# Performance work log

Measured on AMD Instinct MI355X. Metric: run time of the kernel, lower is better.

## Reference

```python
import jax, jax.numpy as jnp
import numpy as np

H = 1024


def _linear(x, W, b):
    # torch nn.Linear: y = x @ W.T + b
    return jnp.einsum('...i,oi->...o', x, W) + b


def setup_inputs() -> dict:
    key = jax.random.key(0)
    ks = jax.random.split(key, 10)
    s = 1.0 / np.sqrt(H)
    inp = {
        'p': jax.random.normal(ks[0], (8, 4096, H), dtype=jnp.float32),
        'x': jax.random.normal(ks[1], (8, 64, H), dtype=jnp.float32),
        'Wq': jax.random.uniform(ks[2], (H, H), jnp.float32, -s, s),
        'bq': jax.random.uniform(ks[3], (H,), jnp.float32, -s, s),
        'Wk': jax.random.uniform(ks[4], (H, H), jnp.float32, -s, s),
        'bk': jax.random.uniform(ks[5], (H,), jnp.float32, -s, s),
        'Wv': jax.random.uniform(ks[6], (H, H), jnp.float32, -s, s),
        'bv': jax.random.uniform(ks[7], (H,), jnp.float32, -s, s),
        'Wg': jax.random.uniform(ks[8], (1, 2 * H), jnp.float32, -s, s),
        'bg': jax.random.uniform(ks[9], (1,), jnp.float32, -s, s),
    }
    return inp


def reference(p, x, Wq, bq, Wk, bk, Wv, bv, Wg, bg):
    q = _linear(p, Wq, bq)            # (B, S, H)
    k = _linear(x, Wk, bk)            # (B, L, H)
    v = _linear(x, Wv, bv)            # (B, L, H)
    # NOTE: scale applied AFTER softmax, faithful to the original module
    scores = jax.nn.softmax(jnp.einsum('bsh,blh->bsl', q, k), axis=-1)
    scores = scores / jnp.sqrt(jnp.asarray(H, p.dtype))
    out = jnp.einsum('bsl,blh->bsh', scores, v) + p
    g = jax.nn.sigmoid(_linear(jnp.concatenate([out, p], axis=2), Wg, bg))  # (B,S,1)
    return g * out + (1.0 - g) * p
```

## Files before the change

### kernel.cpp

```cpp
#include <hip/hip_runtime.h>

#define H 1024
#define SEQ 4096

typedef float f32x4 __attribute__((ext_vector_type(4)));
typedef short s16x8 __attribute__((ext_vector_type(8)));
typedef unsigned short u16;
typedef u16 u16x4 __attribute__((ext_vector_type(4)));
typedef u16 u16x8 __attribute__((ext_vector_type(8)));

__device__ inline u16 f2bf(float f) {
  union { float f; unsigned u; } v; v.f = f;
  unsigned r = v.u + 0x7fffu + ((v.u >> 16) & 1u);
  return (u16)(r >> 16);
}
__device__ inline float bf2f(u16 b) {
  union { unsigned u; float f; } v; v.u = ((unsigned)b) << 16; return v.f;
}

__device__ __forceinline__ void cvt16(const float* __restrict__ src, u16* __restrict__ dst, int i) {
  const float4* s = reinterpret_cast<const float4*>(src) + (size_t)i * 4;
  float4 a = s[0], b = s[1], c = s[2], d = s[3];
  u16x8 lo, hi;
  lo[0]=f2bf(a.x); lo[1]=f2bf(a.y); lo[2]=f2bf(a.z); lo[3]=f2bf(a.w);
  lo[4]=f2bf(b.x); lo[5]=f2bf(b.y); lo[6]=f2bf(b.z); lo[7]=f2bf(b.w);
  hi[0]=f2bf(c.x); hi[1]=f2bf(c.y); hi[2]=f2bf(c.z); hi[3]=f2bf(c.w);
  hi[4]=f2bf(d.x); hi[5]=f2bf(d.y); hi[6]=f2bf(d.z); hi[7]=f2bf(d.w);
  u16x8* o = reinterpret_cast<u16x8*>(dst) + (size_t)i * 2;
  o[0] = lo; o[1] = hi;
}

__global__ __launch_bounds__(256) void prep_kernel(
    const float* __restrict__ Wq, const float* __restrict__ Wk,
    const float* __restrict__ Wv, const float* __restrict__ x,
    const float* __restrict__ Wg,
    u16* __restrict__ wqTb, u16* __restrict__ wkb, u16* __restrict__ wvb,
    u16* __restrict__ xb, float* __restrict__ wgs, float* __restrict__ zeros) {
  __shared__ u16 tls[64][65];
  int blk = blockIdx.x, t = threadIdx.x;
  if (blk < 256) {
    int ti = blk >> 4, tj = blk & 15;
    int lr = t >> 2, cq = (t & 3) * 16;
    const float* s = Wq + (size_t)(ti * 64 + lr) * H + tj * 64 + cq;
#pragma unroll
    for (int q = 0; q < 4; ++q) {
      float4 v = *reinterpret_cast<const float4*>(s + q * 4);
      tls[lr][cq + q * 4 + 0] = f2bf(v.x);
      tls[lr][cq + q * 4 + 1] = f2bf(v.y);
      tls[lr][cq + q * 4 + 2] = f2bf(v.z);
      tls[lr][cq + q * 4 + 3] = f2bf(v.w);
    }
    __syncthreads();
    u16x8 a, b2;
#pragma unroll
    for (int i = 0; i < 8; ++i) a[i] = tls[cq + i][lr];
#pragma unroll
    for (int i = 0; i < 8; ++i) b2[i] = tls[cq + 8 + i][lr];
    u16* d = wqTb + (size_t)(tj * 64 + lr) * H + ti * 64 + cq;
    *reinterpret_cast<u16x8*>(d) = a;
    *reinterpret_cast<u16x8*>(d + 8) = b2;
  } else if (blk < 512) {
    cvt16(Wk, wkb, (blk - 256) * 256 + t);
  } else if (blk < 768) {
    cvt16(Wv, wvb, (blk - 512) * 256 + t);
  } else if (blk < 896) {
    cvt16(x, xb, (blk - 768) * 256 + t);
  } else {
    int i = t * 4;
    float4 a = *reinterpret_cast<const float4*>(Wg + i);
    float4 b2 = *reinterpret_cast<const float4*>(Wg + H + i);
    float4 o; o.x=a.x+b2.x; o.y=a.y+b2.y; o.z=a.z+b2.z; o.w=a.w+b2.w;
    *reinterpret_cast<float4*>(wgs + i) = o;
    float4 z; z.x=0.f; z.y=0.f; z.z=0.f; z.w=0.f;
    *reinterpret_cast<float4*>(zeros + i) = z;
  }
}

__device__ __forceinline__ void gemm_body(const u16* __restrict__ A, const u16* __restrict__ W,
                                          const float* __restrict__ bias, u16* __restrict__ out,
                                          int mt, int nt, int omode, u16* sm) {
  int m0 = mt * 128, n0 = nt * 128;
  int t = threadIdx.x;
  int wave = t >> 6, lane = t & 63;
  int lane15 = lane & 15, lhi = lane >> 4;
  int wr = wave >> 1, wc = wave & 1;
  u16* a_sm = sm;
  u16* b_sm = sm + 8192;

  f32x4 acc[4][4];
#pragma unroll
  for (int mi = 0; mi < 4; ++mi)
#pragma unroll
    for (int ni = 0; ni < 4; ++ni) acc[mi][ni] = (f32x4)0.f;

  int rsel = wave * 32 + (lane >> 3);
  int csel = (lane & 7) * 8;
  const u16* Ab = A + (size_t)m0 * H + csel;
  const u16* Wb = W + (size_t)n0 * H + csel;

  for (int kt = 0; kt < 16; ++kt) {
    int kc = kt * 64;
#pragma unroll
    for (int j = 0; j < 4; ++j) {
      const u16* ga = Ab + (size_t)(rsel + j * 8) * H + kc;
      const u16* gb = Wb + (size_t)(rsel + j * 8) * H + kc;
      __builtin_amdgcn_global_load_lds((const __attribute__((address_space(1))) unsigned int*)ga,
                                       (__attribute__((address_space(3))) unsigned int*)&a_sm[wave * 2048 + j * 512],
                                       16, 0, 0);
      __builtin_amdgcn_global_load_lds((const __attribute__((address_space(1))) unsigned int*)gb,
                                       (__attribute__((address_space(3))) unsigned int*)&b_sm[wave * 2048 + j * 512],
                                       16, 0, 0);
    }
    __syncthreads();
#pragma unroll
    for (int ks = 0; ks < 2; ++ks) {
      s16x8 af[4], bfr[4];
#pragma unroll
      for (int mi = 0; mi < 4; ++mi)
        af[mi] = *reinterpret_cast<const s16x8*>(&a_sm[(wr * 64 + mi * 16 + lane15) * 64 + ks * 32 + lhi * 8]);
#pragma unroll
      for (int ni = 0; ni < 4; ++ni)
        bfr[ni] = *reinterpret_cast<const s16x8*>(&b_sm[(wc * 64 + ni * 16 + lane15) * 64 + ks * 32 + lhi * 8]);
#pragma unroll
      for (int mi = 0; mi < 4; ++mi)
#pragma unroll
        for (int ni = 0; ni < 4; ++ni)
          acc[mi][ni] = __builtin_amdgcn_mfma_f32_16x16x32_bf16(af[mi], bfr[ni], acc[mi][ni], 0, 0, 0);
    }
    __syncthreads();
  }

  float bqv[4];
#pragma unroll
  for (int ni = 0; ni < 4; ++ni) bqv[ni] = bias[n0 + wc * 64 + ni * 16 + lane15];

  if (omode == 0) {
#pragma unroll
    for (int mi = 0; mi < 4; ++mi)
#pragma unroll
      for (int ni = 0; ni < 4; ++ni)
#pragma unroll
        for (int r = 0; r < 4; ++r)
          sm[(wr * 64 + mi * 16 + lhi * 4 + r) * 128 + wc * 64 + ni * 16 + lane15] =
              f2bf(acc[mi][ni][r] + bqv[ni]);
    __syncthreads();
#pragma unroll
    for (int i = 0; i < 4; ++i) {
      int lin2 = i * 4096 + t * 16;
      int row = lin2 >> 7, col = lin2 & 127;
      u16x8 v0 = *reinterpret_cast<const u16x8*>(&sm[lin2]);
      u16x8 v1 = *reinterpret_cast<const u16x8*>(&sm[lin2 + 8]);
      u16* o = out + (size_t)(m0 + row) * H + n0 + col;
      *reinterpret_cast<u16x8*>(o) = v0;
      *reinterpret_cast<u16x8*>(o + 8) = v1;
    }
  } else {
#pragma unroll
    for (int mi = 0; mi < 4; ++mi)
#pragma unroll
      for (int ni = 0; ni < 4; ++ni) {
        int col = n0 + wc * 64 + ni * 16 + lane15;
#pragma unroll
        for (int r = 0; r < 4; ++r) {
          int row = m0 + wr * 64 + mi * 16 + lhi * 4 + r;
          out[((size_t)(row >> 6) * H + col) * 64 + (row & 63)] = f2bf(acc[mi][ni][r] + bqv[ni]);
        }
      }
  }
}

__global__ __launch_bounds__(256) void kv1_kernel(const u16* __restrict__ xb,
                                                  const u16* __restrict__ wkb, const u16* __restrict__ wvb,
                                                  const float* __restrict__ bk, const float* __restrict__ bv,
                                                  u16* __restrict__ kbf, u16* __restrict__ vTb) {
  __shared__ __align__(16) u16 sm[128 * 128];
  int sel = blockIdx.x >> 5;
  int bid = blockIdx.x & 31;
  if (sel == 0)
    gemm_body(xb, wkb, bk, kbf, bid >> 3, bid & 7, 0, sm);
  else
    gemm_body(xb, wvb, bv, vTb, bid >> 3, bid & 7, 2, sm);
}

__global__ __launch_bounds__(256) void kv2_kernel(const u16* __restrict__ kbf,
                                                  const u16* __restrict__ wqTb,
                                                  const float* __restrict__ zeros,
                                                  u16* __restrict__ ktb,
                                                  const u16* __restrict__ vTb,
                                                  const float* __restrict__ Wg,
                                                  const float* __restrict__ bq,
                                                  float* __restrict__ vg, float* __restrict__ bqk) {
  if (blockIdx.x < 32) {
    __shared__ __align__(16) u16 sm[128 * 128];
    gemm_body(kbf, wqTb, zeros, ktb, blockIdx.x >> 3, blockIdx.x & 7, 0, sm);
  } else {
    __shared__ float bq_s[H];
    __shared__ float partial[4][64];
    int b = blockIdx.x - 32, t = threadIdx.x;
    *reinterpret_cast<float4*>(&bq_s[t * 4]) = *reinterpret_cast<const float4*>(bq + t * 4);
    int l = t & 63, part = t >> 6;
    float s = 0.f;
    const u16* vtp = vTb + ((size_t)b * H + part * 256) * 64 + l;
    for (int h = 0; h < 256; ++h) s += bf2f(vtp[h * 64]) * Wg[part * 256 + h];
    partial[part][l] = s;
    __syncthreads();
    if (t < 64) vg[b * 64 + t] = partial[0][t] + partial[1][t] + partial[2][t] + partial[3][t];
    int row = t >> 2, qp = t & 3;
    const u16* kr = kbf + ((size_t)b * 64 + row) * H + qp * 256;
    float sb = 0.f;
    for (int j = 0; j < 256; j += 8) {
      u16x8 v8 = *reinterpret_cast<const u16x8*>(kr + j);
      const float* bqp = &bq_s[qp * 256 + j];
#pragma unroll
      for (int i2 = 0; i2 < 8; ++i2) sb += bf2f(v8[i2]) * bqp[i2];
    }
    sb += __shfl_xor(sb, 1);
    sb += __shfl_xor(sb, 2);
    if (qp == 0) bqk[b * 64 + row] = sb;
  }
}

__global__ __launch_bounds__(256, 4) void attn_kernel(
    const float* __restrict__ p, const u16* __restrict__ ktb,
    const u16* __restrict__ vT, const float* __restrict__ wgs,
    const float* __restrict__ vg, const float* __restrict__ bqk,
    const float* __restrict__ bg, float* __restrict__ out) {
  int t = threadIdx.x;
  int orig = blockIdx.x;
  int lin = (orig & 7) * 128 + (orig >> 3);
  int b = lin >> 7, st = lin & 127;
  size_t gm0 = (size_t)b * SEQ + (size_t)st * 32;
  int wave = t >> 6, lane = t & 63, lane15 = lane & 15, lhi = lane >> 4;

  __shared__ __align__(16) float Sp[4][2048];
  __shared__ __align__(16) u16 P_lds[32 * 72];
  __shared__ float vg_l[64], bq_l[64], pg_part[4][32], gs_l[32];

  if (t < 64) { vg_l[t] = vg[b * 64 + t]; bq_l[t] = bqk[b * 64 + t]; }

  {
    const float* pb = p + (gm0 + lane15) * H;
    const u16* kb = ktb + ((size_t)b * 64 + lane15) * H;
    int kq = wave * 256 + lhi * 8;

    f32x4 acc[2][4];
#pragma unroll
    for (int mi = 0; mi < 2; ++mi)
#pragma unroll
      for (int ni = 0; ni < 4; ++ni) acc[mi][ni] = (f32x4)0.f;
    float pg0 = 0.f, pg1 = 0.f;

#pragma unroll 1
    for (int kt = 0; kt < 8; ++kt) {
      int kc = kq + kt * 32;
      f32x4 p0a = *reinterpret_cast<const f32x4*>(pb + kc);
      f32x4 p0b = *reinterpret_cast<const f32x4*>(pb + kc + 4);
      f32x4 p1a = *reinterpret_cast<const f32x4*>(pb + 16 * H + kc);
      f32x4 p1b = *reinterpret_cast<const f32x4*>(pb + 16 * H + kc + 4);
      s16x8 kf0 = *reinterpret_cast<const s16x8*>(kb + kc);
      s16x8 kf1 = *reinterpret_cast<const s16x8*>(kb + 16 * H + kc);
      s16x8 kf2 = *reinterpret_cast<const s16x8*>(kb + 32 * H + kc);
      s16x8 kf3 = *reinterpret_cast<const s16x8*>(kb + 48 * H + kc);
      f32x4 w0 = *reinterpret_cast<const f32x4*>(wgs + kc);
      f32x4 w1 = *reinterpret_cast<const f32x4*>(wgs + kc + 4);

      s16x8 a0, a1;
      a0[0]=f2bf(p0a[0]); a0[1]=f2bf(p0a[1]); a0[2]=f2bf(p0a[2]); a0[3]=f2bf(p0a[3]);
      a0[4]=f2bf(p0b[0]); a0[5]=f2bf(p0b[1]); a0[6]=f2bf(p0b[2]); a0[7]=f2bf(p0b[3]);
      a1[0]=f2bf(p1a[0]); a1[1]=f2bf(p1a[1]); a1[2]=f2bf(p1a[2]); a1[3]=f2bf(p1a[3]);
      a1[4]=f2bf(p1b[0]); a1[5]=f2bf(p1b[1]); a1[6]=f2bf(p1b[2]); a1[7]=f2bf(p1b[3]);

      acc[0][0] = __builtin_amdgcn_mfma_f32_16x16x32_bf16(a0, kf0, acc[0][0], 0, 0, 0);
      acc[0][1] = __builtin_amdgcn_mfma_f32_16x16x32_bf16(a0, kf1, acc[0][1], 0, 0, 0);
      acc[0][2] = __builtin_amdgcn_mfma_f32_16x16x32_bf16(a0, kf2, acc[0][2], 0, 0, 0);
      acc[0][3] = __builtin_amdgcn_mfma_f32_16x16x32_bf16(a0, kf3, acc[0][3], 0, 0, 0);
      acc[1][0] = __builtin_amdgcn_mfma_f32_16x16x32_bf16(a1, kf0, acc[1][0], 0, 0, 0);
      acc[1][1] = __builtin_amdgcn_mfma_f32_16x16x32_bf16(a1, kf1, acc[1][1], 0, 0, 0);
      acc[1][2] = __builtin_amdgcn_mfma_f32_16x16x32_bf16(a1, kf2, acc[1][2], 0, 0, 0);
      acc[1][3] = __builtin_amdgcn_mfma_f32_16x16x32_bf16(a1, kf3, acc[1][3], 0, 0, 0);

      pg0 += p0a[0]*w0[0] + p0a[1]*w0[1] + p0a[2]*w0[2] + p0a[3]*w0[3]
           + p0b[0]*w1[0] + p0b[1]*w1[1] + p0b[2]*w1[2] + p0b[3]*w1[3];
      pg1 += p1a[0]*w0[0] + p1a[1]*w0[1] + p1a[2]*w0[2] + p1a[3]*w0[3]
           + p1b[0]*w1[0] + p1b[1]*w1[1] + p1b[2]*w1[2] + p1b[3]*w1[3];
    }

    pg0 += __shfl_xor(pg0, 16); pg0 += __shfl_xor(pg0, 32);
    pg1 += __shfl_xor(pg1, 16); pg1 += __shfl_xor(pg1, 32);
    if (lane < 16) { pg_part[wave][lane15] = pg0; pg_part[wave][16 + lane15] = pg1; }

    float* sp = &Sp[wave][0];
#pragma unroll
    for (int mi = 0; mi < 2; ++mi)
#pragma unroll
      for (int ni = 0; ni < 4; ++ni)
#pragma unroll
        for (int r = 0; r < 4; ++r)
          sp[(mi * 16 + lhi * 4 + r) * 64 + ni * 16 + lane15] = acc[mi][ni][r];
  }
  __syncthreads();

  {
    int row = t >> 3, c0 = (t & 7) * 8;
    f32x4 sA = (f32x4)0.f, sB = (f32x4)0.f;
#pragma unroll
    for (int w = 0; w < 4; ++w) {
      sA += *reinterpret_cast<const f32x4*>(&Sp[w][row * 64 + c0]);
      sB += *reinterpret_cast<const f32x4*>(&Sp[w][row * 64 + c0 + 4]);
    }
    float ev[8];
    float se = 0.f, sv = 0.f;
#pragma unroll
    for (int j = 0; j < 4; ++j) {
      float e = __expf(sA[j] + bq_l[c0 + j]);
      ev[j] = e; se += e; sv += e * vg_l[c0 + j];
    }
#pragma unroll
    for (int j = 0; j < 4; ++j) {
      float e = __expf(sB[j] + bq_l[c0 + 4 + j]);
      ev[4 + j] = e; se += e; sv += e * vg_l[c0 + 4 + j];
    }
    se += __shfl_xor(se, 1); se += __shfl_xor(se, 2); se += __shfl_xor(se, 4);
    sv += __shfl_xor(sv, 1); sv += __shfl_xor(sv, 2); sv += __shfl_xor(sv, 4);
    u16x8 pw;
#pragma unroll
    for (int j = 0; j < 8; ++j) pw[j] = f2bf(ev[j]);
    *reinterpret_cast<u16x8*>(&P_lds[row * 72 + c0]) = pw;
    if ((t & 7) == 0) {
      float pg = pg_part[0][row] + pg_part[1][row] + pg_part[2][row] + pg_part[3][row];
      float inv = 1.f / (32.f * se);
      float logit = sv * inv + pg + bg[0];
      gs_l[row] = inv / (1.f + __expf(-logit));
    }
  }
  __syncthreads();

  {
    s16x8 pa[2][2];
#pragma unroll
    for (int mi = 0; mi < 2; ++mi)
#pragma unroll
      for (int ks = 0; ks < 2; ++ks)
        pa[mi][ks] = *reinterpret_cast<const s16x8*>(&P_lds[(mi * 16 + lane15) * 72 + ks * 32 + lhi * 8]);

    const u16* vb = vT + (size_t)b * H * 64;
    float* sc = &Sp[0][0] + wave * 2048;
#pragma unroll
    for (int hcc = 0; hcc < 4; ++hcc) {
      int hbase = wave * 256 + hcc * 64;
      f32x4 acc[2][4];
#pragma unroll
      for (int mi = 0; mi < 2; ++mi)
#pragma unroll
        for (int ni = 0; ni < 4; ++ni) acc[mi][ni] = (f32x4)0.f;
#pragma unroll
      for (int ks = 0; ks < 2; ++ks) {
        s16x8 bv8[4];
#pragma unroll
        for (int ni = 0; ni < 4; ++ni)
          bv8[ni] = *reinterpret_cast<const s16x8*>(vb + (size_t)(hbase + ni * 16 + lane15) * 64 + ks * 32 + lhi * 8);
#pragma unroll
        for (int mi = 0; mi < 2; ++mi)
#pragma unroll
          for (int ni = 0; ni < 4; ++ni)
            acc[mi][ni] = __builtin_amdgcn_mfma_f32_16x16x32_bf16(pa[mi][ks], bv8[ni], acc[mi][ni], 0, 0, 0);
      }
      int swz = (lhi & 1) << 4;
#pragma unroll
      for (int mi = 0; mi < 2; ++mi)
#pragma unroll
        for (int ni = 0; ni < 4; ++ni)
#pragma unroll
          for (int r = 0; r < 4; ++r)
            sc[(mi * 16 + lhi * 4 + r) * 64 + ((ni * 16 + lane15) ^ swz)] = acc[mi][ni][r];
      asm volatile("s_waitcnt lgkmcnt(0)" ::: "memory");
      __builtin_amdgcn_sched_barrier(0);
#pragma unroll
      for (int ii = 0; ii < 8; ++ii) {
        int flat4 = ii * 64 + lane;
        int lrow = flat4 >> 4;
        int c4 = flat4 & 15;
        int scol = (c4 * 4) ^ (((lrow >> 2) & 1) << 4);
        f32x4 a = *reinterpret_cast<const f32x4*>(&sc[lrow * 64 + scol]);
        size_t grow = gm0 + lrow;
        float f = gs_l[lrow];
        float4 pr4 = *reinterpret_cast<const float4*>(&p[grow * H + hbase + c4 * 4]);
        f32x4 o;
        o[0] = pr4.x + f * a[0];
        o[1] = pr4.y + f * a[1];
        o[2] = pr4.z + f * a[2];
        o[3] = pr4.w + f * a[3];
        *reinterpret_cast<f32x4*>(&out[grow * H + hbase + c4 * 4]) = o;
      }
      asm volatile("s_waitcnt lgkmcnt(0)" ::: "memory");
    }
  }
}

extern "C" void kernel_launch(void* const* d_in, const int* in_sizes, int n_in,
                              void* d_out, int out_size, void* d_ws, size_t ws_size,
                              hipStream_t stream) {
  const float* p  = (const float*)d_in[0];
  const float* x  = (const float*)d_in[1];
  const float* Wq = (const float*)d_in[2];
  const float* bq = (const float*)d_in[3];
  const float* Wk = (const float*)d_in[4];
  const float* bk = (const float*)d_in[5];
  const float* Wv = (const float*)d_in[6];
  const float* bv = (const float*)d_in[7];
  const float* Wg = (const float*)d_in[8];
  const float* bg = (const float*)d_in[9];
  float* out = (float*)d_out;

  char* ws = (char*)d_ws;
  u16* wqTb    = (u16*)(ws);
  u16* wkb     = (u16*)(ws + 2097152);
  u16* wvb     = (u16*)(ws + 4194304);
  u16* xb      = (u16*)(ws + 6291456);
  u16* kbf     = (u16*)(ws + 7340032);
  u16* ktb     = (u16*)(ws + 8388608);
  u16* vTb     = (u16*)(ws + 9437184);
  float* wgs   = (float*)(ws + 10485760);
  float* zeros = (float*)(ws + 10489856);
  float* vg    = (float*)(ws + 10493952);
  float* bqk   = (float*)(ws + 10498048);

  prep_kernel<<<897, 256, 0, stream>>>(Wq, Wk, Wv, x, Wg, wqTb, wkb, wvb, xb, wgs, zeros);
  kv1_kernel<<<64, 256, 0, stream>>>(xb, wkb, wvb, bk, bv, kbf, vTb);
  kv2_kernel<<<40, 256, 0, stream>>>(kbf, wqTb, zeros, ktb, vTb, Wg, bq, vg, bqk);
  attn_kernel<<<1024, 256, 0, stream>>>(p, ktb, vTb, wgs, vg, bqk, bg, out);
}
```

Measured before the change: 126.2 us.

## Stage p tile as bf16 in LDS and reuse it for scores, gate, and residual

The attention kernel now processes 16 query rows per block instead of 32 and launches twice as many blocks. Each block loads its p rows once from global memory, converts them to bf16, and keeps them in a swizzled LDS buffer. That buffer feeds the QK MFMA, the gate dot product and the final residual add, removing the second fp32 read of p from global memory. In exchange the residual and gate now use bf16-rounded p, which loses precision. LDS use per block rises and the launch bound drops to 3 blocks per CU.

```diff
diff --git a/kernel.cpp b/kernel.cpp
--- a/kernel.cpp
+++ b/kernel.cpp
@@ -220,114 +220,108 @@
   }
 }
 
-__global__ __launch_bounds__(256, 4) void attn_kernel(
+__global__ __launch_bounds__(256, 3) void attn_kernel(
     const float* __restrict__ p, const u16* __restrict__ ktb,
     const u16* __restrict__ vT, const float* __restrict__ wgs,
     const float* __restrict__ vg, const float* __restrict__ bqk,
     const float* __restrict__ bg, float* __restrict__ out) {
   int t = threadIdx.x;
   int orig = blockIdx.x;
-  int lin = (orig & 7) * 128 + (orig >> 3);
-  int b = lin >> 7, st = lin & 127;
-  size_t gm0 = (size_t)b * SEQ + (size_t)st * 32;
+  int lin = (orig & 7) * 256 + (orig >> 3);
+  int b = lin >> 8, st = lin & 255;
+  size_t gm0 = (size_t)b * SEQ + (size_t)st * 16;
   int wave = t >> 6, lane = t & 63, lane15 = lane & 15, lhi = lane >> 4;
 
-  __shared__ __align__(16) float Sp[4][2048];
-  __shared__ __align__(16) u16 P_lds[32 * 72];
-  __shared__ float vg_l[64], bq_l[64], pg_part[4][32], gs_l[32];
+  __shared__ __align__(16) u16 p_lds[16 * 1024];
+  __shared__ __align__(16) float Sp[4][1024];
+  __shared__ __align__(16) u16 P_lds[16 * 72];
+  __shared__ float vg_l[64], bq_l[64], gs_l[16];
 
   if (t < 64) { vg_l[t] = vg[b * 64 + t]; bq_l[t] = bqk[b * 64 + t]; }
 
   {
-    const float* pb = p + (gm0 + lane15) * H;
-    const u16* kb = ktb + ((size_t)b * 64 + lane15) * H;
-    int kq = wave * 256 + lhi * 8;
-
-    f32x4 acc[2][4];
-#pragma unroll
-    for (int mi = 0; mi < 2; ++mi)
-#pragma unroll
-      for (int ni = 0; ni < 4; ++ni) acc[mi][ni] = (f32x4)0.f;
-    float pg0 = 0.f, pg1 = 0.f;
+    int srow = t >> 7;
+    int scol = t & 127;
+    const float* gp = p + (gm0 + srow) * H + scol * 8;
+    f32x4 r0[8], r1[8];
+#pragma unroll
+    for (int i = 0; i < 8; ++i) {
+      r0[i] = *reinterpret_cast<const f32x4*>(gp + (size_t)(2 * i) * H);
+      r1[i] = *reinterpret_cast<const f32x4*>(gp + (size_t)(2 * i) * H + 4);
+    }
+#pragma unroll
+    for (int i = 0; i < 8; ++i) {
+      int row = 2 * i + srow;
+      u16x8 o;
+      o[0]=f2bf(r0[i][0]); o[1]=f2bf(r0[i][1]); o[2]=f2bf(r0[i][2]); o[3]=f2bf(r0[i][3]);
+      o[4]=f2bf(r1[i][0]); o[5]=f2bf(r1[i][1]); o[6]=f2bf(r1[i][2]); o[7]=f2bf(r1[i][3]);
+      *reinterpret_cast<u16x8*>(&p_lds[row * 1024 + ((scol ^ (row & 7)) << 3)]) = o;
+    }
+  }
+  __syncthreads();
+
+  {
+    const u16* kb = ktb + ((size_t)b * 64 + lane15) * H + lhi * 8;
+    f32x4 acc[4];
+#pragma unroll
+    for (int ni = 0; ni < 4; ++ni) acc[ni] = (f32x4)0.f;
+    int arow = lane15 * 1024;
+    int aswz = lane15 & 7;
 
 #pragma unroll 1
     for (int kt = 0; kt < 8; ++kt) {
-      int kc = kq + kt * 32;
-      f32x4 p0a = *reinterpret_cast<const f32x4*>(pb + kc);
-      f32x4 p0b = *reinterpret_cast<const f32x4*>(pb + kc + 4);
-      f32x4 p1a = *reinterpret_cast<const f32x4*>(pb + 16 * H + kc);
-      f32x4 p1b = *reinterpret_cast<const f32x4*>(pb + 16 * H + kc + 4);
-      s16x8 kf0 = *reinterpret_cast<const s16x8*>(kb + kc);
-      s16x8 kf1 = *reinterpret_cast<const s16x8*>(kb + 16 * H + kc);
-      s16x8 kf2 = *reinterpret_cast<const s16x8*>(kb + 32 * H + kc);
-      s16x8 kf3 = *reinterpret_cast<const s16x8*>(kb + 48 * H + kc);
-      f32x4 w0 = *reinterpret_cast<const f32x4*>(wgs + kc);
-      f32x4 w1 = *reinterpret_cast<const f32x4*>(wgs + kc + 4);
-
-      s16x8 a0, a1;
-      a0[0]=f2bf(p0a[0]); a0[1]=f2bf(p0a[1]); a0[2]=f2bf(p0a[2]); a0[3]=f2bf(p0a[3]);
-      a0[4]=f2bf(p0b[0]); a0[5]=f2bf(p0b[1]); a0[6]=f2bf(p0b[2]); a0[7]=f2bf(p0b[3]);
-      a1[0]=f2bf(p1a[0]); a1[1]=f2bf(p1a[1]); a1[2]=f2bf(p1a[2]); a1[3]=f2bf(p1a[3]);
-      a1[4]=f2bf(p1b[0]); a1[5]=f2bf(p1b[1]); a1[6]=f2bf(p1b[2]); a1[7]=f2bf(p1b[3]);
-
-      acc[0][0] = __builtin_amdgcn_mfma_f32_16x16x32_bf16(a0, kf0, acc[0][0], 0, 0, 0);
-      acc[0][1] = __builtin_amdgcn_mfma_f32_16x16x32_bf16(a0, kf1, acc[0][1], 0, 0, 0);
-      acc[0][2] = __builtin_amdgcn_mfma_f32_16x16x32_bf16(a0, kf2, acc[0][2], 0, 0, 0);
-      acc[0][3] = __builtin_amdgcn_mfma_f32_16x16x32_bf16(a0, kf3, acc[0][3], 0, 0, 0);
-      acc[1][0] = __builtin_amdgcn_mfma_f32_16x16x32_bf16(a1, kf0, acc[1][0], 0, 0, 0);
-      acc[1][1] = __builtin_amdgcn_mfma_f32_16x16x32_bf16(a1, kf1, acc[1][1], 0, 0, 0);
-      acc[1][2] = __builtin_amdgcn_mfma_f32_16x16x32_bf16(a1, kf2, acc[1][2], 0, 0, 0);
-      acc[1][3] = __builtin_amdgcn_mfma_f32_16x16x32_bf16(a1, kf3, acc[1][3], 0, 0, 0);
-
-      pg0 += p0a[0]*w0[0] + p0a[1]*w0[1] + p0a[2]*w0[2] + p0a[3]*w0[3]
-           + p0b[0]*w1[0] + p0b[1]*w1[1] + p0b[2]*w1[2] + p0b[3]*w1[3];
-      pg1 += p1a[0]*w0[0] + p1a[1]*w0[1] + p1a[2]*w0[2] + p1a[3]*w0[3]
-           + p1b[0]*w1[0] + p1b[1]*w1[1] + p1b[2]*w1[2] + p1b[3]*w1[3];
-    }
-
-    pg0 += __shfl_xor(pg0, 16); pg0 += __shfl_xor(pg0, 32);
-    pg1 += __shfl_xor(pg1, 16); pg1 += __shfl_xor(pg1, 32);
-    if (lane < 16) { pg_part[wave][lane15] = pg0; pg_part[wave][16 + lane15] = pg1; }
-
+      int kc = wave * 256 + kt * 32;
+      int sb = (kc >> 3) + lhi;
+      s16x8 a = *reinterpret_cast<const s16x8*>(&p_lds[arow + ((sb ^ aswz) << 3)]);
+      s16x8 k0 = *reinterpret_cast<const s16x8*>(kb + kc);
+      s16x8 k1 = *reinterpret_cast<const s16x8*>(kb + (size_t)16 * H + kc);
+      s16x8 k2 = *reinterpret_cast<const s16x8*>(kb + (size_t)32 * H + kc);
+      s16x8 k3 = *reinterpret_cast<const s16x8*>(kb + (size_t)48 * H + kc);
+      acc[0] = __builtin_amdgcn_mfma_f32_16x16x32_bf16(a, k0, acc[0], 0, 0, 0);
+      acc[1] = __builtin_amdgcn_mfma_f32_16x16x32_bf16(a, k1, acc[1], 0, 0, 0);
+      acc[2] = __builtin_amdgcn_mfma_f32_16x16x32_bf16(a, k2, acc[2], 0, 0, 0);
+      acc[3] = __builtin_amdgcn_mfma_f32_16x16x32_bf16(a, k3, acc[3], 0, 0, 0);
+    }
     float* sp = &Sp[wave][0];
 #pragma unroll
-    for (int mi = 0; mi < 2; ++mi)
-#pragma unroll
-      for (int ni = 0; ni < 4; ++ni)
-#pragma unroll
-        for (int r = 0; r < 4; ++r)
-          sp[(mi * 16 + lhi * 4 + r) * 64 + ni * 16 + lane15] = acc[mi][ni][r];
+    for (int ni = 0; ni < 4; ++ni)
+#pragma unroll
+      for (int r = 0; r < 4; ++r)
+        sp[(lhi * 4 + r) * 64 + ni * 16 + lane15] = acc[ni][r];
   }
   __syncthreads();
 
   {
-    int row = t >> 3, c0 = (t & 7) * 8;
-    f32x4 sA = (f32x4)0.f, sB = (f32x4)0.f;
-#pragma unroll
-    for (int w = 0; w < 4; ++w) {
-      sA += *reinterpret_cast<const f32x4*>(&Sp[w][row * 64 + c0]);
-      sB += *reinterpret_cast<const f32x4*>(&Sp[w][row * 64 + c0 + 4]);
-    }
-    float ev[8];
-    float se = 0.f, sv = 0.f;
+    int row = t >> 4, q = t & 15;
+    int cq = q * 4;
+    f32x4 s4 = *reinterpret_cast<const f32x4*>(&Sp[0][row * 64 + cq]);
+    s4 += *reinterpret_cast<const f32x4*>(&Sp[1][row * 64 + cq]);
+    s4 += *reinterpret_cast<const f32x4*>(&Sp[2][row * 64 + cq]);
+    s4 += *reinterpret_cast<const f32x4*>(&Sp[3][row * 64 + cq]);
+    float ev[4], se = 0.f, sv = 0.f;
 #pragma unroll
     for (int j = 0; j < 4; ++j) {
-      float e = __expf(sA[j] + bq_l[c0 + j]);
-      ev[j] = e; se += e; sv += e * vg_l[c0 + j];
-    }
-#pragma unroll
-    for (int j = 0; j < 4; ++j) {
-      float e = __expf(sB[j] + bq_l[c0 + 4 + j]);
-      ev[4 + j] = e; se += e; sv += e * vg_l[c0 + 4 + j];
-    }
-    se += __shfl_xor(se, 1); se += __shfl_xor(se, 2); se += __shfl_xor(se, 4);
-    sv += __shfl_xor(sv, 1); sv += __shfl_xor(sv, 2); sv += __shfl_xor(sv, 4);
-    u16x8 pw;
-#pragma unroll
-    for (int j = 0; j < 8; ++j) pw[j] = f2bf(ev[j]);
-    *reinterpret_cast<u16x8*>(&P_lds[row * 72 + c0]) = pw;
-    if ((t & 7) == 0) {
-      float pg = pg_part[0][row] + pg_part[1][row] + pg_part[2][row] + pg_part[3][row];
+      float e = __expf(s4[j] + bq_l[cq + j]);
+      ev[j] = e; se += e; sv += e * vg_l[cq + j];
+    }
+    float pg = 0.f;
+    int prow = row * 1024, pswz = row & 7;
+#pragma unroll
+    for (int k8 = 0; k8 < 8; ++k8) {
+      int s = q * 8 + k8;
+      u16x8 pv8 = *reinterpret_cast<const u16x8*>(&p_lds[prow + ((s ^ pswz) << 3)]);
+      const float* w_ = wgs + q * 64 + k8 * 8;
+      pg += bf2f(pv8[0]) * w_[0] + bf2f(pv8[1]) * w_[1] + bf2f(pv8[2]) * w_[2] + bf2f(pv8[3]) * w_[3]
+          + bf2f(pv8[4]) * w_[4] + bf2f(pv8[5]) * w_[5] + bf2f(pv8[6]) * w_[6] + bf2f(pv8[7]) * w_[7];
+    }
+    se += __shfl_xor(se, 1); se += __shfl_xor(se, 2); se += __shfl_xor(se, 4); se += __shfl_xor(se, 8);
+    sv += __shfl_xor(sv, 1); sv += __shfl_xor(sv, 2); sv += __shfl_xor(sv, 4); sv += __shfl_xor(sv, 8);
+    pg += __shfl_xor(pg, 1); pg += __shfl_xor(pg, 2); pg += __shfl_xor(pg, 4); pg += __shfl_xor(pg, 8);
+    u16x4 pw;
+#pragma unroll
+    for (int j = 0; j < 4; ++j) pw[j] = f2bf(ev[j]);
+    *reinterpret_cast<u16x4*>(&P_lds[row * 72 + cq]) = pw;
+    if (q == 0) {
       float inv = 1.f / (32.f * se);
       float logit = sv * inv + pg + bg[0];
       gs_l[row] = inv / (1.f + __expf(-logit));
@@ -336,23 +330,19 @@
   __syncthreads();
 
   {
-    s16x8 pa[2][2];
-#pragma unroll
-    for (int mi = 0; mi < 2; ++mi)
-#pragma unroll
-      for (int ks = 0; ks < 2; ++ks)
-        pa[mi][ks] = *reinterpret_cast<const s16x8*>(&P_lds[(mi * 16 + lane15) * 72 + ks * 32 + lhi * 8]);
+    s16x8 pa[2];
+#pragma unroll
+    for (int ks = 0; ks < 2; ++ks)
+      pa[ks] = *reinterpret_cast<const s16x8*>(&P_lds[lane15 * 72 + ks * 32 + lhi * 8]);
 
     const u16* vb = vT + (size_t)b * H * 64;
-    float* sc = &Sp[0][0] + wave * 2048;
+    float* sc = &Sp[0][0] + wave * 1024;
 #pragma unroll
     for (int hcc = 0; hcc < 4; ++hcc) {
       int hbase = wave * 256 + hcc * 64;
-      f32x4 acc[2][4];
-#pragma unroll
-      for (int mi = 0; mi < 2; ++mi)
-#pragma unroll
-        for (int ni = 0; ni < 4; ++ni) acc[mi][ni] = (f32x4)0.f;
+      f32x4 acc[4];
+#pragma unroll
+      for (int ni = 0; ni < 4; ++ni) acc[ni] = (f32x4)0.f;
 #pragma unroll
       for (int ks = 0; ks < 2; ++ks) {
         s16x8 bv8[4];
@@ -360,37 +350,34 @@
         for (int ni = 0; ni < 4; ++ni)
           bv8[ni] = *reinterpret_cast<const s16x8*>(vb + (size_t)(hbase + ni * 16 + lane15) * 64 + ks * 32 + lhi * 8);
 #pragma unroll
-        for (int mi = 0; mi < 2; ++mi)
-#pragma unroll
-          for (int ni = 0; ni < 4; ++ni)
-            acc[mi][ni] = __builtin_amdgcn_mfma_f32_16x16x32_bf16(pa[mi][ks], bv8[ni], acc[mi][ni], 0, 0, 0);
+        for (int ni = 0; ni < 4; ++ni)
+          acc[ni] = __builtin_amdgcn_mfma_f32_16x16x32_bf16(pa[ks], bv8[ni], acc[ni], 0, 0, 0);
       }
       int swz = (lhi & 1) << 4;
 #pragma unroll
-      for (int mi = 0; mi < 2; ++mi)
-#pragma unroll
-        for (int ni = 0; ni < 4; ++ni)
-#pragma unroll
-          for (int r = 0; r < 4; ++r)
-            sc[(mi * 16 + lhi * 4 + r) * 64 + ((ni * 16 + lane15) ^ swz)] = acc[mi][ni][r];
+      for (int ni = 0; ni < 4; ++ni)
+#pragma unroll
+        for (int r = 0; r < 4; ++r)
+          sc[(lhi * 4 + r) * 64 + ((ni * 16 + lane15) ^ swz)] = acc[ni][r];
       asm volatile("s_waitcnt lgkmcnt(0)" ::: "memory");
       __builtin_amdgcn_sched_barrier(0);
 #pragma unroll
-      for (int ii = 0; ii < 8; ++ii) {
+      for (int ii = 0; ii < 4; ++ii) {
         int flat4 = ii * 64 + lane;
         int lrow = flat4 >> 4;
         int c4 = flat4 & 15;
         int scol = (c4 * 4) ^ (((lrow >> 2) & 1) << 4);
         f32x4 a = *reinterpret_cast<const f32x4*>(&sc[lrow * 64 + scol]);
-        size_t grow = gm0 + lrow;
-        float f = gs_l[lrow];
-        float4 pr4 = *reinterpret_cast<const float4*>(&p[grow * H + hbase + c4 * 4]);
+        int sres = (hbase >> 3) + (c4 >> 1);
+        u16x4 pr = *reinterpret_cast<const u16x4*>(
+            &p_lds[lrow * 1024 + ((sres ^ (lrow & 7)) << 3) + (c4 & 1) * 4]);
+        float g = gs_l[lrow];
         f32x4 o;
-        o[0] = pr4.x + f * a[0];
-        o[1] = pr4.y + f * a[1];
-        o[2] = pr4.z + f * a[2];
-        o[3] = pr4.w + f * a[3];
-        *reinterpret_cast<f32x4*>(&out[grow * H + hbase + c4 * 4]) = o;
+        o[0] = bf2f(pr[0]) + g * a[0];
+        o[1] = bf2f(pr[1]) + g * a[1];
+        o[2] = bf2f(pr[2]) + g * a[2];
+        o[3] = bf2f(pr[3]) + g * a[3];
+        *reinterpret_cast<f32x4*>(&out[(gm0 + lrow) * H + hbase + c4 * 4]) = o;
       }
       asm volatile("s_waitcnt lgkmcnt(0)" ::: "memory");
     }
@@ -428,5 +415,5 @@
   prep_kernel<<<897, 256, 0, stream>>>(Wq, Wk, Wv, x, Wg, wqTb, wkb, wvb, xb, wgs, zeros);
   kv1_kernel<<<64, 256, 0, stream>>>(xb, wkb, wvb, bk, bv, kbf, vTb);
   kv2_kernel<<<40, 256, 0, stream>>>(kbf, wqTb, zeros, ktb, vTb, Wg, bq, vg, bqk);
-  attn_kernel<<<1024, 256, 0, stream>>>(p, ktb, vTb, wgs, vg, bqk, bg, out);
-}
+  attn_kernel<<<2048, 256, 0, stream>>>(p, ktb, vTb, wgs, vg, bqk, bg, out);
+}
```

Measured after the change: 161.3 us. 27.8% more time.

## Split attention kernel into score/softmax kernel and PV/output kernel

Applied to the files above, without the earlier changes.

Splits the fused attention kernel into two launches. The first computes scores, the softmax weights and the gate, writing bf16 probabilities and gate scales to workspace (reusing the wk/xb regions). The second reads them back, runs the PV MFMA and the residual epilogue. The apparent aim is lighter per-kernel resource use, but the 64 MB p tensor is now read twice from HBM and there is extra launch and global round-trip overhead.

```diff
diff --git a/kernel.cpp b/kernel.cpp
--- a/kernel.cpp
+++ b/kernel.cpp
@@ -220,11 +220,11 @@
   }
 }
 
-__global__ __launch_bounds__(256, 4) void attn_kernel(
+__global__ __launch_bounds__(256, 4) void s_kernel(
     const float* __restrict__ p, const u16* __restrict__ ktb,
-    const u16* __restrict__ vT, const float* __restrict__ wgs,
-    const float* __restrict__ vg, const float* __restrict__ bqk,
-    const float* __restrict__ bg, float* __restrict__ out) {
+    const float* __restrict__ wgs, const float* __restrict__ vg,
+    const float* __restrict__ bqk, const float* __restrict__ bg,
+    u16* __restrict__ Pbuf, float* __restrict__ gsbuf) {
   int t = threadIdx.x;
   int orig = blockIdx.x;
   int lin = (orig & 7) * 128 + (orig >> 3);
@@ -233,8 +233,7 @@
   int wave = t >> 6, lane = t & 63, lane15 = lane & 15, lhi = lane >> 4;
 
   __shared__ __align__(16) float Sp[4][2048];
-  __shared__ __align__(16) u16 P_lds[32 * 72];
-  __shared__ float vg_l[64], bq_l[64], pg_part[4][32], gs_l[32];
+  __shared__ float vg_l[64], bq_l[64], pg_part[4][32];
 
   if (t < 64) { vg_l[t] = vg[b * 64 + t]; bq_l[t] = bqk[b * 64 + t]; }
 
@@ -325,75 +324,91 @@
     u16x8 pw;
 #pragma unroll
     for (int j = 0; j < 8; ++j) pw[j] = f2bf(ev[j]);
-    *reinterpret_cast<u16x8*>(&P_lds[row * 72 + c0]) = pw;
+    *reinterpret_cast<u16x8*>(&Pbuf[(size_t)lin * 2048 + row * 64 + c0]) = pw;
     if ((t & 7) == 0) {
       float pg = pg_part[0][row] + pg_part[1][row] + pg_part[2][row] + pg_part[3][row];
       float inv = 1.f / (32.f * se);
       float logit = sv * inv + pg + bg[0];
-      gs_l[row] = inv / (1.f + __expf(-logit));
-    }
-  }
+      gsbuf[lin * 32 + row] = inv / (1.f + __expf(-logit));
+    }
+  }
+}
+
+__global__ __launch_bounds__(256, 4) void pv_kernel(
+    const float* __restrict__ p, const u16* __restrict__ vT,
+    const u16* __restrict__ Pbuf, const float* __restrict__ gsbuf,
+    float* __restrict__ out) {
+  int t = threadIdx.x;
+  int orig = blockIdx.x;
+  int lin = (orig & 7) * 128 + (orig >> 3);
+  int b = lin >> 7, st = lin & 127;
+  size_t gm0 = (size_t)b * SEQ + (size_t)st * 32;
+  int wave = t >> 6, lane = t & 63, lane15 = lane & 15, lhi = lane >> 4;
+
+  __shared__ __align__(16) float sc_all[4][2048];
+  __shared__ float gs_l[32];
+
+  if (t < 32) gs_l[t] = gsbuf[lin * 32 + t];
+
+  s16x8 pa[2][2];
+  const u16* pfb = Pbuf + (size_t)lin * 2048;
+#pragma unroll
+  for (int mi = 0; mi < 2; ++mi)
+#pragma unroll
+    for (int ks = 0; ks < 2; ++ks)
+      pa[mi][ks] = *reinterpret_cast<const s16x8*>(pfb + (mi * 16 + lane15) * 64 + ks * 32 + lhi * 8);
   __syncthreads();
 
-  {
-    s16x8 pa[2][2];
+  const u16* vb = vT + (size_t)b * H * 64;
+  float* sc = &sc_all[wave][0];
+#pragma unroll
+  for (int hcc = 0; hcc < 4; ++hcc) {
+    int hbase = wave * 256 + hcc * 64;
+    f32x4 acc[2][4];
 #pragma unroll
     for (int mi = 0; mi < 2; ++mi)
 #pragma unroll
-      for (int ks = 0; ks < 2; ++ks)
-        pa[mi][ks] = *reinterpret_cast<const s16x8*>(&P_lds[(mi * 16 + lane15) * 72 + ks * 32 + lhi * 8]);
-
-    const u16* vb = vT + (size_t)b * H * 64;
-    float* sc = &Sp[0][0] + wave * 2048;
-#pragma unroll
-    for (int hcc = 0; hcc < 4; ++hcc) {
-      int hbase = wave * 256 + hcc * 64;
-      f32x4 acc[2][4];
+      for (int ni = 0; ni < 4; ++ni) acc[mi][ni] = (f32x4)0.f;
+#pragma unroll
+    for (int ks = 0; ks < 2; ++ks) {
+      s16x8 bv8[4];
+#pragma unroll
+      for (int ni = 0; ni < 4; ++ni)
+        bv8[ni] = *reinterpret_cast<const s16x8*>(vb + (size_t)(hbase + ni * 16 + lane15) * 64 + ks * 32 + lhi * 8);
 #pragma unroll
       for (int mi = 0; mi < 2; ++mi)
 #pragma unroll
-        for (int ni = 0; ni < 4; ++ni) acc[mi][ni] = (f32x4)0.f;
-#pragma unroll
-      for (int ks = 0; ks < 2; ++ks) {
-        s16x8 bv8[4];
-#pragma unroll
         for (int ni = 0; ni < 4; ++ni)
-          bv8[ni] = *reinterpret_cast<const s16x8*>(vb + (size_t)(hbase + ni * 16 + lane15) * 64 + ks * 32 + lhi * 8);
-#pragma unroll
-        for (int mi = 0; mi < 2; ++mi)
-#pragma unroll
-          for (int ni = 0; ni < 4; ++ni)
-            acc[mi][ni] = __builtin_amdgcn_mfma_f32_16x16x32_bf16(pa[mi][ks], bv8[ni], acc[mi][ni], 0, 0, 0);
-      }
-      int swz = (lhi & 1) << 4;
-#pragma unroll
-      for (int mi = 0; mi < 2; ++mi)
-#pragma unroll
-        for (int ni = 0; ni < 4; ++ni)
-#pragma unroll
-          for (int r = 0; r < 4; ++r)
-            sc[(mi * 16 + lhi * 4 + r) * 64 + ((ni * 16 + lane15) ^ swz)] = acc[mi][ni][r];
-      asm volatile("s_waitcnt lgkmcnt(0)" ::: "memory");
-      __builtin_amdgcn_sched_barrier(0);
-#pragma unroll
-      for (int ii = 0; ii < 8; ++ii) {
-        int flat4 = ii * 64 + lane;
-        int lrow = flat4 >> 4;
-        int c4 = flat4 & 15;
-        int scol = (c4 * 4) ^ (((lrow >> 2) & 1) << 4);
-        f32x4 a = *reinterpret_cast<const f32x4*>(&sc[lrow * 64 + scol]);
-        size_t grow = gm0 + lrow;
-        float f = gs_l[lrow];
-        float4 pr4 = *reinterpret_cast<const float4*>(&p[grow * H + hbase + c4 * 4]);
-        f32x4 o;
-        o[0] = pr4.x + f * a[0];
-        o[1] = pr4.y + f * a[1];
-        o[2] = pr4.z + f * a[2];
-        o[3] = pr4.w + f * a[3];
-        *reinterpret_cast<f32x4*>(&out[grow * H + hbase + c4 * 4]) = o;
-      }
-      asm volatile("s_waitcnt lgkmcnt(0)" ::: "memory");
-    }
+          acc[mi][ni] = __builtin_amdgcn_mfma_f32_16x16x32_bf16(pa[mi][ks], bv8[ni], acc[mi][ni], 0, 0, 0);
+    }
+    int swz = (lhi & 1) << 4;
+#pragma unroll
+    for (int mi = 0; mi < 2; ++mi)
+#pragma unroll
+      for (int ni = 0; ni < 4; ++ni)
+#pragma unroll
+        for (int r = 0; r < 4; ++r)
+          sc[(mi * 16 + lhi * 4 + r) * 64 + ((ni * 16 + lane15) ^ swz)] = acc[mi][ni][r];
+    asm volatile("s_waitcnt lgkmcnt(0)" ::: "memory");
+    __builtin_amdgcn_sched_barrier(0);
+#pragma unroll
+    for (int ii = 0; ii < 8; ++ii) {
+      int flat4 = ii * 64 + lane;
+      int lrow = flat4 >> 4;
+      int c4 = flat4 & 15;
+      int scol = (c4 * 4) ^ (((lrow >> 2) & 1) << 4);
+      f32x4 a = *reinterpret_cast<const f32x4*>(&sc[lrow * 64 + scol]);
+      size_t grow = gm0 + lrow;
+      float g = gs_l[lrow];
+      float4 pr4 = *reinterpret_cast<const float4*>(&p[grow * H + hbase + c4 * 4]);
+      f32x4 o;
+      o[0] = pr4.x + g * a[0];
+      o[1] = pr4.y + g * a[1];
+      o[2] = pr4.z + g * a[2];
+      o[3] = pr4.w + g * a[3];
+      *reinterpret_cast<f32x4*>(&out[grow * H + hbase + c4 * 4]) = o;
+    }
+    asm volatile("s_waitcnt lgkmcnt(0)" ::: "memory");
   }
 }
 
@@ -424,9 +439,12 @@
   float* zeros = (float*)(ws + 10489856);
   float* vg    = (float*)(ws + 10493952);
   float* bqk   = (float*)(ws + 10498048);
+  u16* Pbuf    = (u16*)(ws + 2097152);
+  float* gsbuf = (float*)(ws + 6291456);
 
   prep_kernel<<<897, 256, 0, stream>>>(Wq, Wk, Wv, x, Wg, wqTb, wkb, wvb, xb, wgs, zeros);
   kv1_kernel<<<64, 256, 0, stream>>>(xb, wkb, wvb, bk, bv, kbf, vTb);
   kv2_kernel<<<40, 256, 0, stream>>>(kbf, wqTb, zeros, ktb, vTb, Wg, bq, vg, bqk);
-  attn_kernel<<<1024, 256, 0, stream>>>(p, ktb, vTb, wgs, vg, bqk, bg, out);
-}
+  s_kernel<<<1024, 256, 0, stream>>>(p, ktb, wgs, vg, bqk, bg, Pbuf, gsbuf);
+  pv_kernel<<<1024, 256, 0, stream>>>(p, vTb, Pbuf, gsbuf, out);
+}
```

After: 136.7 us. 1.08x slower.
